# Performance work log

Hardware: AMD Instinct MI355X
Metric: run time of the kernel (lower is better)

The kernel has to match this reference:

```python
import jax, jax.numpy as jnp
import numpy as np

B, C, L = 32, 128, 256  # batch, channels (graph nodes), temporal features (= feas)
K = 2  # Chebyshev order (hardcoded in the module)


def setup_inputs() -> dict:
    key = jax.random.key(0)
    k1, k2, k3 = jax.random.split(key, 3)
    x = jax.random.normal(k1, (B, C, L), dtype=jnp.float32)
    a = jax.random.uniform(k2, (C, C), dtype=jnp.float32)  # nn.Parameter(torch.rand)
    Theta = jax.random.normal(k3, (K, L, L), dtype=jnp.float32)  # (k, feas, num_of_filters)
    return {"x": x, "a": a, "Theta": Theta}


def reference(x, a, Theta):
    b, c, l = x.shape
    # pairwise L1 distance over the feature axis: diff[b,i,j] = sum_l |x[b,i,l] - x[b,j,l]|
    diff = jnp.abs(x[:, :, None, :] - x[:, None, :, :]).sum(-1)  # [b,c,c]
    # F.normalize(diff, dim=0): L2-normalize across the batch dimension
    norm = jnp.sqrt((diff * diff).sum(axis=0, keepdims=True))
    diff = diff / jnp.maximum(norm, 1e-12)
    # learned adjacency
    tmpS = jnp.exp(jax.nn.relu((1.0 - diff) * a))        # [b,c,c]
    adj = tmpS / tmpS.sum(axis=1, keepdims=True)
    deg = adj.sum(axis=1)                                 # [b,c]
    I = jnp.eye(c, dtype=x.dtype)
    D = deg[:, :, None] * I                               # diag_embed(deg)
    Lap = D - adj
    lambda_max = 2.0
    L_t = 2.0 * Lap / lambda_max - I                      # scaled Laplacian, [b,c,c]
    cheb = [jnp.broadcast_to(I, (b, c, c)), L_t]
    for i in range(2, K):
        cheb.append(2.0 * L_t * cheb[i - 1] - cheb[i - 2])
    out = jnp.zeros((b, c, Theta.shape[2]), dtype=x.dtype)
    for kk in range(K):
        # rhs = bmm(T_k^T, x): rhs[b,j,l] = sum_i T_k[b,i,j] * x[b,i,l]
        rhs = jnp.einsum('bij,bil->bjl', cheb[kk], x)
        out = out + rhs @ Theta[kk]
    return jax.nn.relu(out)
```

## Files before the change

kernel.cpp:

```cpp
#include <hip/hip_runtime.h>
#include <hip/hip_bf16.h>


#define NB 32
#define NC 128
#define NL 256

typedef short bf16x8 __attribute__((ext_vector_type(8)));
typedef float f32x4 __attribute__((ext_vector_type(4)));

static __device__ __forceinline__ unsigned short f2bf(float f) {
    unsigned u = __builtin_bit_cast(unsigned, f);
    u += 0x7fff + ((u >> 16) & 1);
    return (unsigned short)(u >> 16);
}

__device__ const unsigned char TI36[36] = {0,0,0,0,0,0,0,0, 1,1,1,1,1,1,1, 2,2,2,2,2,2,
                                           3,3,3,3,3, 4,4,4,4, 5,5,5, 6,6, 7};
__device__ const unsigned char TJ36[36] = {0,1,2,3,4,5,6,7, 1,2,3,4,5,6,7, 2,3,4,5,6,7,
                                           3,4,5,6,7, 4,5,6,7, 5,6,7, 6,7, 7};

__global__ __launch_bounds__(256) void k_pre(const float* __restrict__ x,
                                             const float* __restrict__ Theta,
                                             const float* __restrict__ a,
                                             float* __restrict__ diff,
                                             unsigned short* __restrict__ xb,
                                             unsigned short* __restrict__ xbT,
                                             unsigned short* __restrict__ thT2,
                                             float* __restrict__ aT) {
    __shared__ float smem[8592];
    int bid = blockIdx.x;
    int tid = threadIdx.x;

    if (bid < 1152) {
        int b = bid / 36, p = bid - b * 36;
        int i0 = TI36[p] * 16, j0 = TJ36[p] * 16;
        float* xi = smem;
        float* xj = smem + 4160;
        float* sT = smem + 8320;
        const float4* x4 = (const float4*)(x + (size_t)b * NC * NL);
        for (int idx = tid; idx < 16 * 64; idx += 256) {
            int r = idx >> 6, c = idx & 63;
            *(float4*)&xi[r * 260 + c * 4] = x4[(i0 + r) * 64 + c];
            *(float4*)&xj[r * 260 + c * 4] = x4[(j0 + r) * 64 + c];
        }
        __syncthreads();
        int il = tid >> 4, jl = tid & 15;
        float acc = 0.f;
        #pragma unroll 8
        for (int l4 = 0; l4 < 64; ++l4) {
            float4 u = *(const float4*)&xi[il * 260 + l4 * 4];
            float4 v = *(const float4*)&xj[jl * 260 + l4 * 4];
            acc += fabsf(u.x - v.x) + fabsf(u.y - v.y) +
                   fabsf(u.z - v.z) + fabsf(u.w - v.w);
        }
        float* D = diff + (size_t)b * NC * NC;
        D[(i0 + il) * NC + j0 + jl] = acc;
        sT[jl * 17 + il] = acc;
        __syncthreads();
        D[(j0 + il) * NC + i0 + jl] = sT[il * 17 + jl];
    } else if (bid < 1408) {
        int tt = bid - 1152;
        int b = tt >> 3, rem = tt & 7;
        int i0 = (rem >> 2) * 64, l0 = (rem & 3) * 64;
        const float4* x4 = (const float4*)(x + (size_t)b * NC * NL);
        for (int idx = tid; idx < 1024; idx += 256) {
            int r = idx >> 4, c4 = idx & 15;
            *(float4*)&smem[r * 65 + c4 * 4] = x4[(i0 + r) * 64 + (l0 >> 2) + c4];
        }
        __syncthreads();
        for (int idx = tid; idx < 1024; idx += 256) {
            int r = idx >> 4, c4 = idx & 15;
            ushort4 o;
            o.x = f2bf(smem[r * 65 + c4 * 4 + 0]);
            o.y = f2bf(smem[r * 65 + c4 * 4 + 1]);
            o.z = f2bf(smem[r * 65 + c4 * 4 + 2]);
            o.w = f2bf(smem[r * 65 + c4 * 4 + 3]);
            *(ushort4*)(xb + (size_t)b * 32768 + (size_t)(i0 + r) * 256 + l0 + c4 * 4) = o;
            ushort4 p;
            p.x = f2bf(smem[(c4 * 4 + 0) * 65 + r]);
            p.y = f2bf(smem[(c4 * 4 + 1) * 65 + r]);
            p.z = f2bf(smem[(c4 * 4 + 2) * 65 + r]);
            p.w = f2bf(smem[(c4 * 4 + 3) * 65 + r]);
            *(ushort4*)(xbT + (size_t)b * 32768 + (size_t)(l0 + r) * 128 + i0 + c4 * 4) = p;
        }
    } else if (bid < 1440) {
        int tt = bid - 1408;
        int t = tt >> 4, rem = tt & 15;
        int l0 = (rem >> 2) * 64, n0 = (rem & 3) * 64;
        const float4* T4 = (const float4*)(Theta + (size_t)t * 65536);
        for (int idx = tid; idx < 1024; idx += 256) {
            int r = idx >> 4, c4 = idx & 15;
            *(float4*)&smem[r * 65 + c4 * 4] = T4[(l0 + r) * 64 + (n0 >> 2) + c4];
        }
        __syncthreads();
        for (int idx = tid; idx < 1024; idx += 256) {
            int r = idx >> 4, c4 = idx & 15;
            ushort4 o;
            o.x = f2bf(smem[(c4 * 4 + 0) * 65 + r]);
            o.y = f2bf(smem[(c4 * 4 + 1) * 65 + r]);
            o.z = f2bf(smem[(c4 * 4 + 2) * 65 + r]);
            o.w = f2bf(smem[(c4 * 4 + 3) * 65 + r]);
            *(ushort4*)(thT2 + (size_t)(n0 + r) * 512 + t * 256 + l0 + c4 * 4) = o;
        }
    } else {
        int tt = bid - 1440;
        int i0 = (tt >> 1) * 64, j0 = (tt & 1) * 64;
        for (int it = tid; it < 4096; it += 256) {
            int r = it >> 6, c = it & 63;
            smem[r * 65 + c] = a[(i0 + r) * NC + j0 + c];
        }
        __syncthreads();
        for (int it = tid; it < 4096; it += 256) {
            int r = it >> 6, c = it & 63;
            aT[(j0 + r) * NC + i0 + c] = smem[c * 65 + r];
        }
    }
}

__global__ __launch_bounds__(256) void k_mega(const float* __restrict__ diff,
                                              const float* __restrict__ aT,
                                              const unsigned short* __restrict__ xb,
                                              const unsigned short* __restrict__ xbT,
                                              const unsigned short* __restrict__ thT2,
                                              float* __restrict__ out) {
    __shared__ __align__(16) short adjL[16 * 144];
    __shared__ __align__(16) short yL[16 * 272];
    int bid = blockIdx.x;
    int b = bid >> 3, jt = bid & 7, j0 = jt * 16;
    int tid = threadIdx.x;

    {
        int jl = tid >> 4, il = tid & 15;
        const float* Dp = diff + (size_t)(j0 + jl) * NC + il;
        const float* Ap = aT + (size_t)(j0 + jl) * NC + il;
        float sv[8];
        float cs = 0.f;
        #pragma unroll
        for (int r = 0; r < 8; ++r) {
            int off = 16 * r;
            float ss = 0.f;
            #pragma unroll
            for (int bb = 0; bb < NB; ++bb) {
                float v = Dp[(size_t)bb * NC * NC + off];
                ss = fmaf(v, v, ss);
            }
            float rn = 1.0f / fmaxf(sqrtf(ss), 1e-12f);
            float d  = Dp[(size_t)b * NC * NC + off];
            float av = Ap[off];
            float s = __expf(fmaxf((1.0f - d * rn) * av, 0.0f));
            sv[r] = s;
            cs += s;
        }
        cs += __shfl_xor(cs, 1); cs += __shfl_xor(cs, 2);
        cs += __shfl_xor(cs, 4); cs += __shfl_xor(cs, 8);
        float inv = -1.0f / cs;
        #pragma unroll
        for (int r = 0; r < 8; ++r)
            adjL[jl * 144 + il + 16 * r] = (short)f2bf(sv[r] * inv);
    }
    __syncthreads();

    int w = tid >> 6, lane = tid & 63, lr = lane & 15, lg = lane >> 4;

    {
        f32x4 acc[4];
        #pragma unroll
        for (int f = 0; f < 4; ++f) acc[f] = (f32x4){0.f, 0.f, 0.f, 0.f};
        const unsigned short* Bb = xbT + (size_t)b * 32768;
        #pragma unroll
        for (int ks = 0; ks < 4; ++ks) {
            bf16x8 af = *(const bf16x8*)&adjL[lr * 144 + ks * 32 + lg * 8];
            #pragma unroll
            for (int f = 0; f < 4; ++f) {
                bf16x8 bv = *(const bf16x8*)(Bb + (size_t)(w * 64 + f * 16 + lr) * 128 + ks * 32 + lg * 8);
                acc[f] = __builtin_amdgcn_mfma_f32_16x16x32_bf16(af, bv, acc[f], 0, 0, 0);
            }
        }
        #pragma unroll
        for (int f = 0; f < 4; ++f)
            #pragma unroll
            for (int r = 0; r < 4; ++r)
                yL[(lg * 4 + r) * 272 + w * 64 + f * 16 + lr] = (short)f2bf(acc[f][r]);
    }
    __syncthreads();

    {
        f32x4 o[4];
        #pragma unroll
        for (int f = 0; f < 4; ++f) o[f] = (f32x4){0.f, 0.f, 0.f, 0.f};
        const unsigned short* Arow = xb + (size_t)b * 32768 + (size_t)(j0 + lr) * 256;
        #pragma unroll
        for (int ks = 0; ks < 16; ++ks) {
            bf16x8 af = (ks < 8)
                ? *(const bf16x8*)(Arow + ks * 32 + lg * 8)
                : *(const bf16x8*)&yL[lr * 272 + (ks - 8) * 32 + lg * 8];
            #pragma unroll
            for (int f = 0; f < 4; ++f) {
                bf16x8 bv = *(const bf16x8*)(thT2 + (size_t)(w * 64 + f * 16 + lr) * 512 + ks * 32 + lg * 8);
                o[f] = __builtin_amdgcn_mfma_f32_16x16x32_bf16(af, bv, o[f], 0, 0, 0);
            }
        }
        float* Ob = out + (size_t)b * 32768;
        #pragma unroll
        for (int f = 0; f < 4; ++f)
            #pragma unroll
            for (int r = 0; r < 4; ++r)
                Ob[(size_t)(j0 + lg * 4 + r) * 256 + w * 64 + f * 16 + lr] = fmaxf(o[f][r], 0.f);
    }
}

extern "C" void kernel_launch(void* const* d_in, const int* in_sizes, int n_in,
                              void* d_out, int out_size, void* d_ws, size_t ws_size,
                              hipStream_t stream) {
    const float* x     = (const float*)d_in[0];
    const float* a     = (const float*)d_in[1];
    const float* Theta = (const float*)d_in[2];
    float* out = (float*)d_out;
    float* f0  = (float*)d_ws;

    float*          diff = f0;
    float*          aT   = f0 + 524288;
    unsigned short* xb   = (unsigned short*)(f0 + 540672);
    unsigned short* xbT  = (unsigned short*)(f0 + 1064960);
    unsigned short* thT2 = (unsigned short*)(f0 + 1589248);

    k_pre <<<dim3(1444), dim3(256), 0, stream>>>(x, Theta, a, diff, xb, xbT, thT2, aT);
    k_mega<<<dim3(256), dim3(256), 0, stream>>>(diff, aT, xb, xbT, thT2, out);
}
```

Baseline: 99.55 us.

## Accumulate batch norm via atomics and split adjacency into separate kernel

```diff
diff --git a/kernel.cpp b/kernel.cpp
--- a/kernel.cpp
+++ b/kernel.cpp
@@ -24,6 +24,7 @@
                                              const float* __restrict__ Theta,
                                              const float* __restrict__ a,
                                              float* __restrict__ diff,
+                                             float* __restrict__ ssum,
                                              unsigned short* __restrict__ xb,
                                              unsigned short* __restrict__ xbT,
                                              unsigned short* __restrict__ thT2,
@@ -57,6 +58,9 @@
         float* D = diff + (size_t)b * NC * NC;
         D[(i0 + il) * NC + j0 + jl] = acc;
         sT[jl * 17 + il] = acc;
+        float d2 = acc * acc;
+        atomicAdd(&ssum[(i0 + il) * NC + j0 + jl], d2);
+        if (i0 != j0) atomicAdd(&ssum[(j0 + jl) * NC + i0 + il], d2);
         __syncthreads();
         D[(j0 + il) * NC + i0 + jl] = sT[il * 17 + jl];
     } else if (bid < 1408) {
@@ -118,59 +122,49 @@
     }
 }
 
-__global__ __launch_bounds__(256) void k_mega(const float* __restrict__ diff,
-                                              const float* __restrict__ aT,
+__global__ __launch_bounds__(128) void k_adj(const float* __restrict__ diff,
+                                             const float* __restrict__ ssum,
+                                             const float* __restrict__ aT,
+                                             unsigned short* __restrict__ adjTb) {
+    int bid = blockIdx.x;
+    int b = bid >> 7, j = bid & 127;
+    int i = threadIdx.x;
+    float ss = ssum[j * NC + i];
+    float rn = 1.0f / fmaxf(sqrtf(ss), 1e-12f);
+    float d  = diff[(size_t)b * NC * NC + j * NC + i];
+    float av = aT[j * NC + i];
+    float s = __expf(fmaxf((1.0f - d * rn) * av, 0.0f));
+    float t = s;
+    #pragma unroll
+    for (int off = 32; off; off >>= 1) t += __shfl_xor(t, off);
+    __shared__ float partial[2];
+    if ((i & 63) == 0) partial[i >> 6] = t;
+    __syncthreads();
+    float total = partial[0] + partial[1];
+    adjTb[(size_t)b * NC * NC + j * NC + i] = f2bf(-s / total);
+}
+
+__global__ __launch_bounds__(256) void k_gemm(const unsigned short* __restrict__ adjTb,
                                               const unsigned short* __restrict__ xb,
                                               const unsigned short* __restrict__ xbT,
                                               const unsigned short* __restrict__ thT2,
                                               float* __restrict__ out) {
-    __shared__ __align__(16) short adjL[16 * 144];
     __shared__ __align__(16) short yL[16 * 272];
     int bid = blockIdx.x;
-    int b = bid >> 3, jt = bid & 7, j0 = jt * 16;
-    int tid = threadIdx.x;
-
-    {
-        int jl = tid >> 4, il = tid & 15;
-        const float* Dp = diff + (size_t)(j0 + jl) * NC + il;
-        const float* Ap = aT + (size_t)(j0 + jl) * NC + il;
-        float sv[8];
-        float cs = 0.f;
-        #pragma unroll
-        for (int r = 0; r < 8; ++r) {
-            int off = 16 * r;
-            float ss = 0.f;
-            #pragma unroll
-            for (int bb = 0; bb < NB; ++bb) {
-                float v = Dp[(size_t)bb * NC * NC + off];
-                ss = fmaf(v, v, ss);
-            }
-            float rn = 1.0f / fmaxf(sqrtf(ss), 1e-12f);
-            float d  = Dp[(size_t)b * NC * NC + off];
-            float av = Ap[off];
-            float s = __expf(fmaxf((1.0f - d * rn) * av, 0.0f));
-            sv[r] = s;
-            cs += s;
-        }
-        cs += __shfl_xor(cs, 1); cs += __shfl_xor(cs, 2);
-        cs += __shfl_xor(cs, 4); cs += __shfl_xor(cs, 8);
-        float inv = -1.0f / cs;
-        #pragma unroll
-        for (int r = 0; r < 8; ++r)
-            adjL[jl * 144 + il + 16 * r] = (short)f2bf(sv[r] * inv);
-    }
-    __syncthreads();
-
-    int w = tid >> 6, lane = tid & 63, lr = lane & 15, lg = lane >> 4;
+    int b = bid >> 4, jt = (bid >> 1) & 7, nh = bid & 1;
+    int j0 = jt * 16;
+    int tid = threadIdx.x, w = tid >> 6, lane = tid & 63;
+    int lr = lane & 15, lg = lane >> 4;
 
     {
         f32x4 acc[4];
         #pragma unroll
         for (int f = 0; f < 4; ++f) acc[f] = (f32x4){0.f, 0.f, 0.f, 0.f};
+        const unsigned short* An = adjTb + (size_t)b * 16384 + (size_t)(j0 + lr) * 128 + lg * 8;
         const unsigned short* Bb = xbT + (size_t)b * 32768;
         #pragma unroll
         for (int ks = 0; ks < 4; ++ks) {
-            bf16x8 af = *(const bf16x8*)&adjL[lr * 144 + ks * 32 + lg * 8];
+            bf16x8 af = *(const bf16x8*)(An + ks * 32);
             #pragma unroll
             for (int f = 0; f < 4; ++f) {
                 bf16x8 bv = *(const bf16x8*)(Bb + (size_t)(w * 64 + f * 16 + lr) * 128 + ks * 32 + lg * 8);
@@ -186,9 +180,9 @@
     __syncthreads();
 
     {
-        f32x4 o[4];
-        #pragma unroll
-        for (int f = 0; f < 4; ++f) o[f] = (f32x4){0.f, 0.f, 0.f, 0.f};
+        f32x4 o[2];
+        o[0] = (f32x4){0.f, 0.f, 0.f, 0.f};
+        o[1] = (f32x4){0.f, 0.f, 0.f, 0.f};
         const unsigned short* Arow = xb + (size_t)b * 32768 + (size_t)(j0 + lr) * 256;
         #pragma unroll
         for (int ks = 0; ks < 16; ++ks) {
@@ -196,17 +190,19 @@
                 ? *(const bf16x8*)(Arow + ks * 32 + lg * 8)
                 : *(const bf16x8*)&yL[lr * 272 + (ks - 8) * 32 + lg * 8];
             #pragma unroll
-            for (int f = 0; f < 4; ++f) {
-                bf16x8 bv = *(const bf16x8*)(thT2 + (size_t)(w * 64 + f * 16 + lr) * 512 + ks * 32 + lg * 8);
+            for (int f = 0; f < 2; ++f) {
+                int n = nh * 128 + w * 32 + f * 16 + lr;
+                bf16x8 bv = *(const bf16x8*)(thT2 + (size_t)n * 512 + ks * 32 + lg * 8);
                 o[f] = __builtin_amdgcn_mfma_f32_16x16x32_bf16(af, bv, o[f], 0, 0, 0);
             }
         }
         float* Ob = out + (size_t)b * 32768;
         #pragma unroll
-        for (int f = 0; f < 4; ++f)
+        for (int f = 0; f < 2; ++f)
             #pragma unroll
             for (int r = 0; r < 4; ++r)
-                Ob[(size_t)(j0 + lg * 4 + r) * 256 + w * 64 + f * 16 + lr] = fmaxf(o[f][r], 0.f);
+                Ob[(size_t)(j0 + lg * 4 + r) * 256 + nh * 128 + w * 32 + f * 16 + lr] =
+                    fmaxf(o[f][r], 0.f);
     }
 }
 
@@ -219,12 +215,16 @@
     float* out = (float*)d_out;
     float* f0  = (float*)d_ws;
 
-    float*          diff = f0;
-    float*          aT   = f0 + 524288;
-    unsigned short* xb   = (unsigned short*)(f0 + 540672);
-    unsigned short* xbT  = (unsigned short*)(f0 + 1064960);
-    unsigned short* thT2 = (unsigned short*)(f0 + 1589248);
-
-    k_pre <<<dim3(1444), dim3(256), 0, stream>>>(x, Theta, a, diff, xb, xbT, thT2, aT);
-    k_mega<<<dim3(256), dim3(256), 0, stream>>>(diff, aT, xb, xbT, thT2, out);
-}
+    float*          diff  = f0;
+    float*          ssum  = f0 + 524288;
+    float*          aT    = f0 + 540672;
+    unsigned short* xb    = (unsigned short*)(f0 + 557056);
+    unsigned short* xbT   = (unsigned short*)(f0 + 1081344);
+    unsigned short* thT2  = (unsigned short*)(f0 + 1605632);
+    unsigned short* adjTb = (unsigned short*)(f0 + 1671168);
+
+    hipMemsetAsync(ssum, 0, 16384 * sizeof(float), stream);
+    k_pre <<<dim3(1444), dim3(256), 0, stream>>>(x, Theta, a, diff, ssum, xb, xbT, thT2, aT);
+    k_adj <<<dim3(NB * NC), dim3(128), 0, stream>>>(diff, ssum, aT, adjTb);
+    k_gemm<<<dim3(512), dim3(256), 0, stream>>>(adjTb, xb, xbT, thT2, out);
+}
```

After: 94.34 us. 1.06x faster.

## Precompute batch-norm sums via atomics, enlarge distance tiles, split output columns

Applied to the files above, without the earlier changes.

```diff
diff --git a/kernel.cpp b/kernel.cpp
--- a/kernel.cpp
+++ b/kernel.cpp
@@ -15,52 +15,83 @@
     return (unsigned short)(u >> 16);
 }
 
-__device__ const unsigned char TI36[36] = {0,0,0,0,0,0,0,0, 1,1,1,1,1,1,1, 2,2,2,2,2,2,
-                                           3,3,3,3,3, 4,4,4,4, 5,5,5, 6,6, 7};
-__device__ const unsigned char TJ36[36] = {0,1,2,3,4,5,6,7, 1,2,3,4,5,6,7, 2,3,4,5,6,7,
-                                           3,4,5,6,7, 4,5,6,7, 5,6,7, 6,7, 7};
+__device__ const unsigned char TI10[10] = {0,0,0,0, 1,1,1, 2,2, 3};
+__device__ const unsigned char TJ10[10] = {0,1,2,3, 1,2,3, 2,3, 3};
 
 __global__ __launch_bounds__(256) void k_pre(const float* __restrict__ x,
                                              const float* __restrict__ Theta,
                                              const float* __restrict__ a,
                                              float* __restrict__ diff,
+                                             float* __restrict__ ssum,
                                              unsigned short* __restrict__ xb,
                                              unsigned short* __restrict__ xbT,
                                              unsigned short* __restrict__ thT2,
                                              float* __restrict__ aT) {
-    __shared__ float smem[8592];
+    __shared__ float smem[4480];
     int bid = blockIdx.x;
     int tid = threadIdx.x;
 
-    if (bid < 1152) {
-        int b = bid / 36, p = bid - b * 36;
-        int i0 = TI36[p] * 16, j0 = TJ36[p] * 16;
+    if (bid < 320) {
+        int b = bid / 10, p = bid - b * 10;
+        int i0 = TI10[p] * 32, j0 = TJ10[p] * 32;
         float* xi = smem;
-        float* xj = smem + 4160;
-        float* sT = smem + 8320;
+        float* xj = smem + 2176;
         const float4* x4 = (const float4*)(x + (size_t)b * NC * NL);
-        for (int idx = tid; idx < 16 * 64; idx += 256) {
-            int r = idx >> 6, c = idx & 63;
-            *(float4*)&xi[r * 260 + c * 4] = x4[(i0 + r) * 64 + c];
-            *(float4*)&xj[r * 260 + c * 4] = x4[(j0 + r) * 64 + c];
-        }
-        __syncthreads();
         int il = tid >> 4, jl = tid & 15;
-        float acc = 0.f;
-        #pragma unroll 8
-        for (int l4 = 0; l4 < 64; ++l4) {
-            float4 u = *(const float4*)&xi[il * 260 + l4 * 4];
-            float4 v = *(const float4*)&xj[jl * 260 + l4 * 4];
-            acc += fabsf(u.x - v.x) + fabsf(u.y - v.y) +
-                   fabsf(u.z - v.z) + fabsf(u.w - v.w);
+        float a00 = 0.f, a01 = 0.f, a10 = 0.f, a11 = 0.f;
+        #pragma unroll
+        for (int q = 0; q < 4; ++q) {
+            __syncthreads();
+            #pragma unroll
+            for (int k = 0; k < 2; ++k) {
+                int idx = tid + k * 256;
+                int r = idx >> 4, c4 = idx & 15;
+                *(float4*)&xi[r * 68 + c4 * 4] = x4[(i0 + r) * 64 + q * 16 + c4];
+                *(float4*)&xj[r * 68 + c4 * 4] = x4[(j0 + r) * 64 + q * 16 + c4];
+            }
+            __syncthreads();
+            #pragma unroll
+            for (int l4 = 0; l4 < 16; ++l4) {
+                float4 u0 = *(const float4*)&xi[il * 68 + l4 * 4];
+                float4 u1 = *(const float4*)&xi[(il + 16) * 68 + l4 * 4];
+                float4 v0 = *(const float4*)&xj[jl * 68 + l4 * 4];
+                float4 v1 = *(const float4*)&xj[(jl + 16) * 68 + l4 * 4];
+                a00 += fabsf(u0.x-v0.x)+fabsf(u0.y-v0.y)+fabsf(u0.z-v0.z)+fabsf(u0.w-v0.w);
+                a01 += fabsf(u0.x-v1.x)+fabsf(u0.y-v1.y)+fabsf(u0.z-v1.z)+fabsf(u0.w-v1.w);
+                a10 += fabsf(u1.x-v0.x)+fabsf(u1.y-v0.y)+fabsf(u1.z-v0.z)+fabsf(u1.w-v0.w);
+                a11 += fabsf(u1.x-v1.x)+fabsf(u1.y-v1.y)+fabsf(u1.z-v1.z)+fabsf(u1.w-v1.w);
+            }
         }
         float* D = diff + (size_t)b * NC * NC;
-        D[(i0 + il) * NC + j0 + jl] = acc;
-        sT[jl * 17 + il] = acc;
-        __syncthreads();
-        D[(j0 + il) * NC + i0 + jl] = sT[il * 17 + jl];
-    } else if (bid < 1408) {
-        int tt = bid - 1152;
+        D[(i0 + il) * NC + j0 + jl]           = a00;
+        D[(i0 + il) * NC + j0 + jl + 16]      = a01;
+        D[(i0 + il + 16) * NC + j0 + jl]      = a10;
+        D[(i0 + il + 16) * NC + j0 + jl + 16] = a11;
+        atomicAdd(&ssum[(i0 + il) * NC + j0 + jl],           a00 * a00);
+        atomicAdd(&ssum[(i0 + il) * NC + j0 + jl + 16],      a01 * a01);
+        atomicAdd(&ssum[(i0 + il + 16) * NC + j0 + jl],      a10 * a10);
+        atomicAdd(&ssum[(i0 + il + 16) * NC + j0 + jl + 16], a11 * a11);
+        if (i0 != j0) {
+            atomicAdd(&ssum[(j0 + jl) * NC + i0 + il],           a00 * a00);
+            atomicAdd(&ssum[(j0 + jl + 16) * NC + i0 + il],      a01 * a01);
+            atomicAdd(&ssum[(j0 + jl) * NC + i0 + il + 16],      a10 * a10);
+            atomicAdd(&ssum[(j0 + jl + 16) * NC + i0 + il + 16], a11 * a11);
+            float* sT = smem;
+            __syncthreads();
+            sT[jl * 33 + il]             = a00;
+            sT[(jl + 16) * 33 + il]      = a01;
+            sT[jl * 33 + il + 16]        = a10;
+            sT[(jl + 16) * 33 + il + 16] = a11;
+            __syncthreads();
+            #pragma unroll
+            for (int k = 0; k < 4; ++k) {
+                int idx = tid + k * 256;
+                int r = idx >> 5, c = idx & 31;
+                D[(j0 + r) * NC + i0 + c] = sT[r * 33 + c];
+            }
+        }
+    } else if (bid < 576) {
+        int tt = bid - 320;
         int b = tt >> 3, rem = tt & 7;
         int i0 = (rem >> 2) * 64, l0 = (rem & 3) * 64;
         const float4* x4 = (const float4*)(x + (size_t)b * NC * NL);
@@ -84,8 +115,8 @@
             p.w = f2bf(smem[(c4 * 4 + 3) * 65 + r]);
             *(ushort4*)(xbT + (size_t)b * 32768 + (size_t)(l0 + r) * 128 + i0 + c4 * 4) = p;
         }
-    } else if (bid < 1440) {
-        int tt = bid - 1408;
+    } else if (bid < 608) {
+        int tt = bid - 576;
         int t = tt >> 4, rem = tt & 15;
         int l0 = (rem >> 2) * 64, n0 = (rem & 3) * 64;
         const float4* T4 = (const float4*)(Theta + (size_t)t * 65536);
@@ -104,7 +135,7 @@
             *(ushort4*)(thT2 + (size_t)(n0 + r) * 512 + t * 256 + l0 + c4 * 4) = o;
         }
     } else {
-        int tt = bid - 1440;
+        int tt = bid - 608;
         int i0 = (tt >> 1) * 64, j0 = (tt & 1) * 64;
         for (int it = tid; it < 4096; it += 256) {
             int r = it >> 6, c = it & 63;
@@ -118,7 +149,8 @@
     }
 }
 
-__global__ __launch_bounds__(256) void k_mega(const float* __restrict__ diff,
+__global__ __launch_bounds__(256) void k_fuse(const float* __restrict__ diff,
+                                              const float* __restrict__ ssum,
                                               const float* __restrict__ aT,
                                               const unsigned short* __restrict__ xb,
                                               const unsigned short* __restrict__ xbT,
@@ -127,28 +159,22 @@
     __shared__ __align__(16) short adjL[16 * 144];
     __shared__ __align__(16) short yL[16 * 272];
     int bid = blockIdx.x;
-    int b = bid >> 3, jt = bid & 7, j0 = jt * 16;
+    int b = bid >> 4, jt = (bid >> 1) & 7, nh = bid & 1;
+    int j0 = jt * 16;
     int tid = threadIdx.x;
 
     {
-        int jl = tid >> 4, il = tid & 15;
-        const float* Dp = diff + (size_t)(j0 + jl) * NC + il;
-        const float* Ap = aT + (size_t)(j0 + jl) * NC + il;
+        int jl = tid >> 4, ig = tid & 15;
+        const float* Dp = diff + (size_t)b * NC * NC + (size_t)(j0 + jl) * NC + ig;
+        const float* Sp = ssum + (size_t)(j0 + jl) * NC + ig;
+        const float* Ap = aT   + (size_t)(j0 + jl) * NC + ig;
         float sv[8];
         float cs = 0.f;
         #pragma unroll
         for (int r = 0; r < 8; ++r) {
             int off = 16 * r;
-            float ss = 0.f;
-            #pragma unroll
-            for (int bb = 0; bb < NB; ++bb) {
-                float v = Dp[(size_t)bb * NC * NC + off];
-                ss = fmaf(v, v, ss);
-            }
-            float rn = 1.0f / fmaxf(sqrtf(ss), 1e-12f);
-            float d  = Dp[(size_t)b * NC * NC + off];
-            float av = Ap[off];
-            float s = __expf(fmaxf((1.0f - d * rn) * av, 0.0f));
+            float rn = 1.0f / fmaxf(sqrtf(Sp[off]), 1e-12f);
+            float s = __expf(fmaxf((1.0f - Dp[off] * rn) * Ap[off], 0.0f));
             sv[r] = s;
             cs += s;
         }
@@ -157,7 +183,7 @@
         float inv = -1.0f / cs;
         #pragma unroll
         for (int r = 0; r < 8; ++r)
-            adjL[jl * 144 + il + 16 * r] = (short)f2bf(sv[r] * inv);
+            adjL[jl * 144 + ig + 16 * r] = (short)f2bf(sv[r] * inv);
     }
     __syncthreads();
 
@@ -186,9 +212,9 @@
     __syncthreads();
 
     {
-        f32x4 o[4];
-        #pragma unroll
-        for (int f = 0; f < 4; ++f) o[f] = (f32x4){0.f, 0.f, 0.f, 0.f};
+        f32x4 o[2];
+        o[0] = (f32x4){0.f, 0.f, 0.f, 0.f};
+        o[1] = (f32x4){0.f, 0.f, 0.f, 0.f};
         const unsigned short* Arow = xb + (size_t)b * 32768 + (size_t)(j0 + lr) * 256;
         #pragma unroll
         for (int ks = 0; ks < 16; ++ks) {
@@ -196,17 +222,19 @@
                 ? *(const bf16x8*)(Arow + ks * 32 + lg * 8)
                 : *(const bf16x8*)&yL[lr * 272 + (ks - 8) * 32 + lg * 8];
             #pragma unroll
-            for (int f = 0; f < 4; ++f) {
-                bf16x8 bv = *(const bf16x8*)(thT2 + (size_t)(w * 64 + f * 16 + lr) * 512 + ks * 32 + lg * 8);
+            for (int f = 0; f < 2; ++f) {
+                int n = nh * 128 + w * 32 + f * 16 + lr;
+                bf16x8 bv = *(const bf16x8*)(thT2 + (size_t)n * 512 + ks * 32 + lg * 8);
                 o[f] = __builtin_amdgcn_mfma_f32_16x16x32_bf16(af, bv, o[f], 0, 0, 0);
             }
         }
         float* Ob = out + (size_t)b * 32768;
         #pragma unroll
-        for (int f = 0; f < 4; ++f)
+        for (int f = 0; f < 2; ++f)
             #pragma unroll
             for (int r = 0; r < 4; ++r)
-                Ob[(size_t)(j0 + lg * 4 + r) * 256 + w * 64 + f * 16 + lr] = fmaxf(o[f][r], 0.f);
+                Ob[(size_t)(j0 + lg * 4 + r) * 256 + nh * 128 + w * 32 + f * 16 + lr] =
+                    fmaxf(o[f][r], 0.f);
     }
 }
 
@@ -219,12 +247,14 @@
     float* out = (float*)d_out;
     float* f0  = (float*)d_ws;
 
-    float*          diff = f0;
-    float*          aT   = f0 + 524288;
-    unsigned short* xb   = (unsigned short*)(f0 + 540672);
-    unsigned short* xbT  = (unsigned short*)(f0 + 1064960);
-    unsigned short* thT2 = (unsigned short*)(f0 + 1589248);
-
-    k_pre <<<dim3(1444), dim3(256), 0, stream>>>(x, Theta, a, diff, xb, xbT, thT2, aT);
-    k_mega<<<dim3(256), dim3(256), 0, stream>>>(diff, aT, xb, xbT, thT2, out);
-}
+    float*          diff  = f0;
+    float*          ssum  = f0 + 524288;
+    float*          aT    = f0 + 540672;
+    unsigned short* xb    = (unsigned short*)(f0 + 557056);
+    unsigned short* xbT   = (unsigned short*)(f0 + 1081344);
+    unsigned short* thT2  = (unsigned short*)(f0 + 1605632);
+
+    hipMemsetAsync(ssum, 0, 16384 * sizeof(float), stream);
+    k_pre <<<dim3(612), dim3(256), 0, stream>>>(x, Theta, a, diff, ssum, xb, xbT, thT2, aT);
+    k_fuse<<<dim3(512), dim3(256), 0, stream>>>(diff, ssum, aT, xb, xbT, thT2, out);
+}
```

Measured after the change: 91.13 us (median of 2 runs). -8.5%, faster.
